# Optimization experiments

Measured on AMD Instinct MI355X. Metric: run time of the kernel, lower is better.

## Reference

```python
import jax, jax.numpy as jnp
import numpy as np

EMBED = 256
HEADS = 8
HEAD_DIM = EMBED // HEADS
K = 7          # kernel_size
DIL = 1        # dilation
PAD = DIL * (K - 1) // 2  # 3
B, H, W = 4, 56, 56


def setup_inputs() -> dict:
    key = jax.random.key(0)
    ks = jax.random.split(key, 9)
    d = {"x": jax.random.normal(ks[0], (B, H, W, EMBED), jnp.float32)}
    for i, name in enumerate(["wq", "wk", "wv", "wo"]):
        d[name] = jax.random.normal(ks[1 + i], (EMBED, EMBED), jnp.float32) * 0.02
    for i, name in enumerate(["bq", "bk", "bv", "bo"]):
        d[name] = jax.random.normal(ks[5 + i], (EMBED,), jnp.float32) * 0.02
    return d


def _unfold(t):
    # t: [N, d, H, W] -> [N, d, K*K, H, W]; zero padding (matches F.unfold),
    # so out-of-bounds neighbors contribute logit 0, NOT -inf (faithful to source).
    h, w = t.shape[2], t.shape[3]
    tp = jnp.pad(t, ((0, 0), (0, 0), (PAD, PAD), (PAD, PAD)))
    patches = [tp[:, :, i * DIL:i * DIL + h, j * DIL:j * DIL + w]
               for i in range(K) for j in range(K)]  # fixed K*K=49 offsets
    return jnp.stack(patches, axis=2)


def reference(x, wq, bq, wk, bk, wv, bv, wo, bo):
    b, h, w, c = x.shape
    scale = HEAD_DIM ** -0.5
    q = x @ wq.T + bq
    k = x @ wk.T + bk
    v = x @ wv.T + bv

    def to_nh(t):  # [B,H,W,C] -> [B*heads, head_dim, H, W]
        return t.reshape(b, h, w, HEADS, HEAD_DIM).transpose(0, 3, 4, 1, 2).reshape(b * HEADS, HEAD_DIM, h, w)

    q, k, v = to_nh(q), to_nh(k), to_nh(v)
    k_unf = _unfold(k)  # [N, d, K2, H, W]
    v_unf = _unfold(v)
    logits = jnp.einsum('ndhw,ndkhw->nkhw', q, k_unf) * scale  # [N, K2, H, W]
    attn = jax.nn.softmax(logits, axis=1)
    out = jnp.einsum('nkhw,ndkhw->ndhw', attn, v_unf)  # [N, d, H, W]
    out = out.reshape(b, HEADS, HEAD_DIM, h, w).transpose(0, 3, 4, 1, 2).reshape(b, h, w, c)
    return out @ wo.T + bo
```

## Files before the change

### kernel.cpp

```cpp
#include <hip/hip_runtime.h>

typedef unsigned int u32;
typedef unsigned short u16;
typedef __attribute__((ext_vector_type(8))) short bf16x8;
typedef __attribute__((ext_vector_type(4))) float f32x4;

#define T_TOK 12544
#define EMB   256
#define IMG   56
#define SCALE 0.17677669529663689f
#define HALO  196
#define KSTR  40
#define VTSTR 224
#define PSTR  232

__device__ __forceinline__ u32 bf16_rtne(float f) {
    u32 u = __builtin_bit_cast(u32, f);
    return (u + 0x7fffu + ((u >> 16) & 1u)) >> 16;
}
__device__ __forceinline__ float bf16_to_f(u32 h) { return __builtin_bit_cast(float, h << 16); }
__device__ __forceinline__ u32 pk2(float a, float b) {
    return bf16_rtne(a) | (bf16_rtne(b) << 16);
}

#define GLD16(g, l) __builtin_amdgcn_global_load_lds( \
    (const __attribute__((address_space(1))) u32*)(g), \
    (__attribute__((address_space(3))) u32*)(l), 16, 0, 0)

__global__ __launch_bounds__(256) void weight_convert(
    const float* __restrict__ wq, const float* __restrict__ wk,
    const float* __restrict__ wv, const float* __restrict__ wo,
    u16* __restrict__ bsh, u16* __restrict__ boh, u16* __restrict__ bol) {
    const int i = blockIdx.x * 256 + threadIdx.x;
    const int w = i >> 14, widx = i & 16383;
    const float* src = (w == 0) ? wq : (w == 1) ? wk : (w == 2) ? wv : wo;
    const float4 f = ((const float4*)src)[widx];
    const float vf[4] = {f.x, f.y, f.z, f.w};
    if (w < 3) {
        ushort4 hv;
        u16* hp = (u16*)&hv;
        #pragma unroll
        for (int c = 0; c < 4; ++c) hp[c] = (u16)bf16_rtne(vf[c]);
        ((ushort4*)bsh)[(w << 14) + widx] = hv;
    } else {
        ushort4 hv, lv;
        u16* hp = (u16*)&hv; u16* lp = (u16*)&lv;
        #pragma unroll
        for (int c = 0; c < 4; ++c) {
            const u32 h = bf16_rtne(vf[c]);
            hp[c] = (u16)h;
            lp[c] = (u16)bf16_rtne(vf[c] - bf16_to_f(h));
        }
        ((ushort4*)boh)[widx] = hv;
        ((ushort4*)bol)[widx] = lv;
    }
}

__global__ __launch_bounds__(256) void qkv_mfma(
    const float* __restrict__ x, const u16* __restrict__ bsh,
    const float* __restrict__ bq, const float* __restrict__ bk, const float* __restrict__ bv,
    u16* __restrict__ qb, u16* __restrict__ kb, u16* __restrict__ vb) {
    __shared__ __attribute__((aligned(16))) u16 sA[128 * 32];
    __shared__ __attribute__((aligned(16))) u16 sB[128 * 32];
    const int nBase = blockIdx.x * 128;
    const int mBase = blockIdx.y * 128;
    const int tid = threadIdx.x, wv = tid >> 6, ln = tid & 63;
    const int lrow = ln & 15, lqd = ln >> 4;
    const int wm = (wv & 1) * 64, wn = (wv >> 1) * 64;
    const int c0 = wv * 128 + ln, r0 = c0 >> 2, kc0 = c0 & 3;
    const int c1 = c0 + 64,       r1 = c1 >> 2, kc1 = c1 & 3;
    const size_t gA0 = (size_t)(mBase + r0) * EMB + kc0 * 8;
    const size_t gA1 = (size_t)(mBase + r1) * EMB + kc1 * 8;
    const size_t gB0 = (size_t)(nBase + r0) * EMB + kc0 * 8;
    const size_t gB1 = (size_t)(nBase + r1) * EMB + kc1 * 8;
    const int l0 = (wv * 128) * 8, l1 = (wv * 128 + 64) * 8;

    f32x4 acc[4][4];
    #pragma unroll
    for (int mi = 0; mi < 4; ++mi)
        #pragma unroll
        for (int ni = 0; ni < 4; ++ni)
            acc[mi][ni] = (f32x4){0.f, 0.f, 0.f, 0.f};

    for (int kt = 0; kt < 8; ++kt) {
        const int k0 = kt * 32;
        GLD16(bsh + gB0 + k0, sB + l0);
        GLD16(bsh + gB1 + k0, sB + l1);
        {
            const float4 f0 = *(const float4*)&x[gA0 + k0];
            const float4 f1 = *(const float4*)&x[gA0 + k0 + 4];
            const uint4 p = {pk2(f0.x, f0.y), pk2(f0.z, f0.w),
                             pk2(f1.x, f1.y), pk2(f1.z, f1.w)};
            *(uint4*)&sA[c0 * 8] = p;
        }
        {
            const float4 f0 = *(const float4*)&x[gA1 + k0];
            const float4 f1 = *(const float4*)&x[gA1 + k0 + 4];
            const uint4 p = {pk2(f0.x, f0.y), pk2(f0.z, f0.w),
                             pk2(f1.x, f1.y), pk2(f1.z, f1.w)};
            *(uint4*)&sA[c1 * 8] = p;
        }
        __syncthreads();
        bf16x8 af[4], bf[4];
        #pragma unroll
        for (int mi = 0; mi < 4; ++mi)
            af[mi] = *(const bf16x8*)&sA[(wm + mi * 16 + lrow) * 32 + lqd * 8];
        #pragma unroll
        for (int ni = 0; ni < 4; ++ni)
            bf[ni] = *(const bf16x8*)&sB[(wn + ni * 16 + lrow) * 32 + lqd * 8];
        #pragma unroll
        for (int mi = 0; mi < 4; ++mi)
            #pragma unroll
            for (int ni = 0; ni < 4; ++ni)
                acc[mi][ni] = __builtin_amdgcn_mfma_f32_16x16x32_bf16(af[mi], bf[ni], acc[mi][ni], 0, 0, 0);
        __syncthreads();
    }

    const int which = nBase >> 8;
    const float* bias = (which == 0) ? bq : (which == 1) ? bk : bv;
    u16* dst = (which == 0) ? qb : (which == 1) ? kb : vb;
    #pragma unroll
    for (int ni = 0; ni < 4; ++ni) {
        const int ncol = nBase + wn + ni * 16 + lrow;
        const int c = ncol & 255;
        const float bz = bias[c];
        #pragma unroll
        for (int mi = 0; mi < 4; ++mi) {
            #pragma unroll
            for (int r = 0; r < 4; ++r) {
                const int row = mBase + wm + mi * 16 + lqd * 4 + r;
                dst[(size_t)row * EMB + c] = (u16)bf16_rtne(acc[mi][ni][r] + bz);
            }
        }
    }
}

__global__ __launch_bounds__(256) void out_mfma(
    const u16* __restrict__ aoh, const u16* __restrict__ aol,
    const u16* __restrict__ boh, const u16* __restrict__ bol,
    const float* __restrict__ bo, float* __restrict__ out) {
    __shared__ __attribute__((aligned(16))) u16 sAh[64 * 32];
    __shared__ __attribute__((aligned(16))) u16 sAl[64 * 32];
    __shared__ __attribute__((aligned(16))) u16 sBh[64 * 32];
    __shared__ __attribute__((aligned(16))) u16 sBl[64 * 32];
    const int nBase = blockIdx.x * 64;
    const int mBase = blockIdx.y * 64;
    const int tid = threadIdx.x, wv = tid >> 6, ln = tid & 63;
    const int lrow = ln & 15, lqd = ln >> 4;
    const int rA = tid >> 2, kcA = tid & 3;
    const size_t gA = (size_t)(mBase + rA) * EMB + kcA * 8;
    const size_t gB = (size_t)(nBase + rA) * EMB + kcA * 8;
    const int lA = wv * 64 * 8;

    f32x4 acc[4];
    #pragma unroll
    for (int mi = 0; mi < 4; ++mi) acc[mi] = (f32x4){0.f, 0.f, 0.f, 0.f};

    for (int kt = 0; kt < 8; ++kt) {
        const int k0 = kt * 32;
        GLD16(aoh + gA + k0, sAh + lA);
        GLD16(aol + gA + k0, sAl + lA);
        GLD16(boh + gB + k0, sBh + lA);
        GLD16(bol + gB + k0, sBl + lA);
        __syncthreads();
        bf16x8 ah[4], al[4];
        #pragma unroll
        for (int mi = 0; mi < 4; ++mi) {
            ah[mi] = *(const bf16x8*)&sAh[(mi * 16 + lrow) * 32 + lqd * 8];
            al[mi] = *(const bf16x8*)&sAl[(mi * 16 + lrow) * 32 + lqd * 8];
        }
        const bf16x8 bh = *(const bf16x8*)&sBh[(wv * 16 + lrow) * 32 + lqd * 8];
        const bf16x8 bl = *(const bf16x8*)&sBl[(wv * 16 + lrow) * 32 + lqd * 8];
        #pragma unroll
        for (int mi = 0; mi < 4; ++mi) {
            acc[mi] = __builtin_amdgcn_mfma_f32_16x16x32_bf16(ah[mi], bh, acc[mi], 0, 0, 0);
            acc[mi] = __builtin_amdgcn_mfma_f32_16x16x32_bf16(al[mi], bh, acc[mi], 0, 0, 0);
            acc[mi] = __builtin_amdgcn_mfma_f32_16x16x32_bf16(ah[mi], bl, acc[mi], 0, 0, 0);
        }
        __syncthreads();
    }

    const int ncol = nBase + wv * 16 + lrow;
    const float bz = bo[ncol];
    #pragma unroll
    for (int mi = 0; mi < 4; ++mi) {
        #pragma unroll
        for (int r = 0; r < 4; ++r) {
            const int row = mBase + mi * 16 + lqd * 4 + r;
            out[(size_t)row * EMB + ncol] = acc[mi][r] + bz;
        }
    }
}

__global__ __launch_bounds__(256, 3) void attn_kernel(
    const u16* __restrict__ qb, const u16* __restrict__ kb, const u16* __restrict__ vb,
    u16* __restrict__ aoh, u16* __restrict__ aol) {
    __shared__ __attribute__((aligned(16))) u16 smem[25088];
    u16* sK  = smem;
    u16* sV1 = smem + 8960;
    u16* sVT = smem + 17920;
    u16* sP  = smem;

    const int tid = threadIdx.x;
    const int w = tid >> 6, ln = tid & 63;
    const int lrow = ln & 15, lqd = ln >> 4;
    const int img = blockIdx.z >> 3, head = blockIdx.z & 7;
    const int ty0 = blockIdx.y * 8, tx0 = blockIdx.x * 8;

    for (int i = tid; i < 1792; i += 256) {
        const int mv = (i >= 896) ? 1 : 0;
        const int ii = i - 896 * mv;
        const int p = ii >> 2, c = ii & 3;
        const int pyh = p / 14, pxh = p - pyh * 14;
        const int gy = ty0 - 3 + pyh, gx = tx0 - 3 + pxh;
        u16* dst = (mv ? sV1 : sK) + p * KSTR + c * 8;
        if (p < HALO && (unsigned)gy < 56u && (unsigned)gx < 56u) {
            const size_t tt = ((size_t)img * IMG + gy) * IMG + gx;
            *(uint4*)dst = *(const uint4*)((mv ? vb : kb) + tt * EMB + head * 32 + c * 8);
        } else {
            *(uint4*)dst = (uint4){0u, 0u, 0u, 0u};
        }
    }
    __syncthreads();

    for (int i = tid; i < 896; i += 256) {
        const int d = i & 31, ho = i >> 5;
        u32 pk[4];
        #pragma unroll
        for (int j = 0; j < 4; ++j) {
            const u32 a = sV1[(ho * 8 + 2 * j)     * KSTR + d];
            const u32 b = sV1[(ho * 8 + 2 * j + 1) * KSTR + d];
            pk[j] = a | (b << 16);
        }
        *(uint4*)&sVT[d * VTSTR + ho * 8] = *(uint4*)pk;
    }

    const int mpix = w * 16 + lrow;
    const int qpy = mpix >> 3, qpx = mpix & 7;
    const size_t qtok = ((size_t)img * IMG + ty0 + qpy) * IMG + tx0 + qpx;
    const bf16x8 aq = *(const bf16x8*)&qb[qtok * EMB + head * 32 + lqd * 8];

    f32x4 ct[13];
    #pragma unroll
    for (int t = 0; t < 13; ++t) ct[t] = (f32x4){0.f, 0.f, 0.f, 0.f};
    #pragma unroll
    for (int t = 0; t < 13; ++t) {
        const bf16x8 bk = *(const bf16x8*)&sK[(t * 16 + lrow) * KSTR + lqd * 8];
        ct[t] = __builtin_amdgcn_mfma_f32_16x16x32_bf16(aq, bk, ct[t], 0, 0, 0);
    }

    int pys[4], pxs[4];
    #pragma unroll
    for (int r = 0; r < 4; ++r) {
        const int row = lqd * 4 + r;
        pys[r] = 2 * w + (row >> 3);
        pxs[r] = row & 7;
    }
    float mr4[4] = {-1e30f, -1e30f, -1e30f, -1e30f};
    #pragma unroll
    for (int t = 0; t < 13; ++t) {
        const int col = t * 16 + lrow;
        const int hy = col / 14, hx = col - 14 * hy;
        const bool okc = (col < HALO);
        #pragma unroll
        for (int r = 0; r < 4; ++r) {
            const bool ok = ((unsigned)(hy - pys[r]) < 7u) &
                            ((unsigned)(hx - pxs[r]) < 7u) & okc;
            const float lv = ok ? ct[t][r] * SCALE : -1e30f;
            ct[t][r] = lv;
            mr4[r] = fmaxf(mr4[r], lv);
        }
    }
    #pragma unroll
    for (int r = 0; r < 4; ++r) {
        float m = mr4[r];
        m = fmaxf(m, __shfl_xor(m, 1));
        m = fmaxf(m, __shfl_xor(m, 2));
        m = fmaxf(m, __shfl_xor(m, 4));
        m = fmaxf(m, __shfl_xor(m, 8));
        mr4[r] = m;
    }
    float sr4[4] = {0.f, 0.f, 0.f, 0.f};
    #pragma unroll
    for (int t = 0; t < 13; ++t)
        #pragma unroll
        for (int r = 0; r < 4; ++r) {
            const float e = __expf(ct[t][r] - mr4[r]);
            ct[t][r] = e;
            sr4[r] += e;
        }
    #pragma unroll
    for (int r = 0; r < 4; ++r) {
        float s = sr4[r];
        s += __shfl_xor(s, 1);
        s += __shfl_xor(s, 2);
        s += __shfl_xor(s, 4);
        s += __shfl_xor(s, 8);
        sr4[r] = 1.0f / s;
    }

    __syncthreads();

    u16* sPw = sP + w * 16 * PSTR;
    #pragma unroll
    for (int t = 0; t < 13; ++t)
        #pragma unroll
        for (int r = 0; r < 4; ++r)
            sPw[(lqd * 4 + r) * PSTR + t * 16 + lrow] = (u16)bf16_rtne(ct[t][r]);
    #pragma unroll
    for (int z = 0; z < 4; ++z) {
        const int idx = z * 64 + ln;
        sPw[(idx >> 4) * PSTR + 208 + (idx & 15)] = 0;
    }

    f32x4 o0 = (f32x4){0.f, 0.f, 0.f, 0.f};
    f32x4 o1 = (f32x4){0.f, 0.f, 0.f, 0.f};
    #pragma unroll
    for (int ks = 0; ks < 7; ++ks) {
        const bf16x8 ap  = *(const bf16x8*)&sPw[lrow * PSTR + ks * 32 + lqd * 8];
        const bf16x8 bv0 = *(const bf16x8*)&sVT[lrow * VTSTR + ks * 32 + lqd * 8];
        const bf16x8 bv1 = *(const bf16x8*)&sVT[(16 + lrow) * VTSTR + ks * 32 + lqd * 8];
        o0 = __builtin_amdgcn_mfma_f32_16x16x32_bf16(ap, bv0, o0, 0, 0, 0);
        o1 = __builtin_amdgcn_mfma_f32_16x16x32_bf16(ap, bv1, o1, 0, 0, 0);
    }

    #pragma unroll
    for (int r = 0; r < 4; ++r) {
        const int row = lqd * 4 + r;
        const int opy = 2 * w + (row >> 3), opx = row & 7;
        const size_t ot = ((size_t)img * IMG + ty0 + opy) * IMG + tx0 + opx;
        const float inv = sr4[r];
        const float v0 = o0[r] * inv;
        const float v1 = o1[r] * inv;
        const size_t base = ot * EMB + head * 32;
        const u32 h0 = bf16_rtne(v0);
        aoh[base + lrow] = (u16)h0;
        aol[base + lrow] = (u16)bf16_rtne(v0 - bf16_to_f(h0));
        const u32 h1 = bf16_rtne(v1);
        aoh[base + 16 + lrow] = (u16)h1;
        aol[base + 16 + lrow] = (u16)bf16_rtne(v1 - bf16_to_f(h1));
    }
}

extern "C" void kernel_launch(void* const* d_in, const int* in_sizes, int n_in,
                              void* d_out, int out_size, void* d_ws, size_t ws_size,
                              hipStream_t stream) {
    const float* x  = (const float*)d_in[0];
    const float* wq = (const float*)d_in[1];
    const float* wk = (const float*)d_in[2];
    const float* wv = (const float*)d_in[3];
    const float* wo = (const float*)d_in[4];
    const float* bq = (const float*)d_in[5];
    const float* bk = (const float*)d_in[6];
    const float* bv = (const float*)d_in[7];
    const float* bo = (const float*)d_in[8];
    float* out = (float*)d_out;

    char* ws = (char*)d_ws;
    u16* qb  = (u16*)(ws);
    u16* kb  = (u16*)(ws +  6422528);
    u16* vb  = (u16*)(ws + 12845056);
    u16* aoh = (u16*)(ws + 19267584);
    u16* aol = (u16*)(ws + 25690112);
    u16* bsh = (u16*)(ws + 32112640);
    u16* boh = (u16*)(ws + 32505856);
    u16* bol = (u16*)(ws + 32636928);

    weight_convert<<<256, 256, 0, stream>>>(wq, wk, wv, wo, bsh, boh, bol);
    qkv_mfma<<<dim3(6, 98), 256, 0, stream>>>(x, bsh, bq, bk, bv, qb, kb, vb);
    attn_kernel<<<dim3(7, 7, 32), 256, 0, stream>>>(qb, kb, vb, aoh, aol);
    out_mfma<<<dim3(4, 196), 256, 0, stream>>>(aoh, aol, boh, bol, bo, out);
}
```

Baseline: 133.8 us.

## Pre-convert x to bf16 and double-buffer GEMM LDS tiles

The convert kernel now also casts x to bf16 into a workspace buffer, so the QKV GEMM can stream A tiles with direct global-to-LDS loads instead of loading fp32 and packing in registers. Both GEMMs use double-buffered shared memory, prefetching the next K-slice while computing the current one, which removes one barrier per iteration. The attention kernel writes V transposed straight into LDS during the halo load, dropping a separate transpose pass and a barrier. The cost is an extra full pass over x (an 6.4MB bf16 write plus its read back) and scattered 16-bit LDS stores for the V transpose.

Result: no change. 134.0 us (+0.2%).

```diff
diff --git a/kernel.cpp b/kernel.cpp
--- a/kernel.cpp
+++ b/kernel.cpp
@@ -19,61 +19,71 @@
     return (u + 0x7fffu + ((u >> 16) & 1u)) >> 16;
 }
 __device__ __forceinline__ float bf16_to_f(u32 h) { return __builtin_bit_cast(float, h << 16); }
-__device__ __forceinline__ u32 pk2(float a, float b) {
-    return bf16_rtne(a) | (bf16_rtne(b) << 16);
-}
 
 #define GLD16(g, l) __builtin_amdgcn_global_load_lds( \
     (const __attribute__((address_space(1))) u32*)(g), \
     (__attribute__((address_space(3))) u32*)(l), 16, 0, 0)
 
-__global__ __launch_bounds__(256) void weight_convert(
-    const float* __restrict__ wq, const float* __restrict__ wk,
+__global__ __launch_bounds__(256) void convert_kernel(
+    const float* __restrict__ x, const float* __restrict__ wq, const float* __restrict__ wk,
     const float* __restrict__ wv, const float* __restrict__ wo,
-    u16* __restrict__ bsh, u16* __restrict__ boh, u16* __restrict__ bol) {
+    u16* __restrict__ xb, u16* __restrict__ bsh,
+    u16* __restrict__ boh, u16* __restrict__ bol) {
     const int i = blockIdx.x * 256 + threadIdx.x;
-    const int w = i >> 14, widx = i & 16383;
-    const float* src = (w == 0) ? wq : (w == 1) ? wk : (w == 2) ? wv : wo;
-    const float4 f = ((const float4*)src)[widx];
-    const float vf[4] = {f.x, f.y, f.z, f.w};
-    if (w < 3) {
+    const int NX4 = T_TOK * EMB / 4;
+    if (i < NX4) {
+        const float4 f = ((const float4*)x)[i];
+        const float vf[4] = {f.x, f.y, f.z, f.w};
         ushort4 hv;
         u16* hp = (u16*)&hv;
         #pragma unroll
         for (int c = 0; c < 4; ++c) hp[c] = (u16)bf16_rtne(vf[c]);
-        ((ushort4*)bsh)[(w << 14) + widx] = hv;
+        ((ushort4*)xb)[i] = hv;
     } else {
-        ushort4 hv, lv;
-        u16* hp = (u16*)&hv; u16* lp = (u16*)&lv;
-        #pragma unroll
-        for (int c = 0; c < 4; ++c) {
-            const u32 h = bf16_rtne(vf[c]);
-            hp[c] = (u16)h;
-            lp[c] = (u16)bf16_rtne(vf[c] - bf16_to_f(h));
-        }
-        ((ushort4*)boh)[widx] = hv;
-        ((ushort4*)bol)[widx] = lv;
+        const int j = i - NX4;
+        const int w = j >> 14, widx = j & 16383;
+        const float* src = (w == 0) ? wq : (w == 1) ? wk : (w == 2) ? wv : wo;
+        const float4 f = ((const float4*)src)[widx];
+        const float vf[4] = {f.x, f.y, f.z, f.w};
+        if (w < 3) {
+            ushort4 hv;
+            u16* hp = (u16*)&hv;
+            #pragma unroll
+            for (int c = 0; c < 4; ++c) hp[c] = (u16)bf16_rtne(vf[c]);
+            ((ushort4*)bsh)[(w << 14) + widx] = hv;
+        } else {
+            ushort4 hv, lv;
+            u16* hp = (u16*)&hv; u16* lp = (u16*)&lv;
+            #pragma unroll
+            for (int c = 0; c < 4; ++c) {
+                const u32 h = bf16_rtne(vf[c]);
+                hp[c] = (u16)h;
+                lp[c] = (u16)bf16_rtne(vf[c] - bf16_to_f(h));
+            }
+            ((ushort4*)boh)[widx] = hv;
+            ((ushort4*)bol)[widx] = lv;
+        }
     }
 }
 
 __global__ __launch_bounds__(256) void qkv_mfma(
-    const float* __restrict__ x, const u16* __restrict__ bsh,
+    const u16* __restrict__ xb, const u16* __restrict__ bsh,
     const float* __restrict__ bq, const float* __restrict__ bk, const float* __restrict__ bv,
     u16* __restrict__ qb, u16* __restrict__ kb, u16* __restrict__ vb) {
-    __shared__ __attribute__((aligned(16))) u16 sA[128 * 32];
-    __shared__ __attribute__((aligned(16))) u16 sB[128 * 32];
+    __shared__ __attribute__((aligned(16))) u16 sA[2][128 * 32];
+    __shared__ __attribute__((aligned(16))) u16 sB[2][128 * 32];
     const int nBase = blockIdx.x * 128;
     const int mBase = blockIdx.y * 128;
-    const int tid = threadIdx.x, wv = tid >> 6, ln = tid & 63;
+    const int tid = threadIdx.x, wv2 = tid >> 6, ln = tid & 63;
     const int lrow = ln & 15, lqd = ln >> 4;
-    const int wm = (wv & 1) * 64, wn = (wv >> 1) * 64;
-    const int c0 = wv * 128 + ln, r0 = c0 >> 2, kc0 = c0 & 3;
-    const int c1 = c0 + 64,       r1 = c1 >> 2, kc1 = c1 & 3;
+    const int wm = (wv2 & 1) * 64, wn = (wv2 >> 1) * 64;
+    const int c0 = wv2 * 128 + ln, r0 = c0 >> 2, kc0 = c0 & 3;
+    const int c1 = c0 + 64,        r1 = c1 >> 2, kc1 = c1 & 3;
     const size_t gA0 = (size_t)(mBase + r0) * EMB + kc0 * 8;
     const size_t gA1 = (size_t)(mBase + r1) * EMB + kc1 * 8;
     const size_t gB0 = (size_t)(nBase + r0) * EMB + kc0 * 8;
     const size_t gB1 = (size_t)(nBase + r1) * EMB + kc1 * 8;
-    const int l0 = (wv * 128) * 8, l1 = (wv * 128 + 64) * 8;
+    const int l0 = (wv2 * 128) * 8, l1 = (wv2 * 128 + 64) * 8;
 
     f32x4 acc[4][4];
     #pragma unroll
@@ -82,38 +92,33 @@
         for (int ni = 0; ni < 4; ++ni)
             acc[mi][ni] = (f32x4){0.f, 0.f, 0.f, 0.f};
 
+    GLD16(xb  + gA0, &sA[0][l0]);
+    GLD16(xb  + gA1, &sA[0][l1]);
+    GLD16(bsh + gB0, &sB[0][l0]);
+    GLD16(bsh + gB1, &sB[0][l1]);
+
     for (int kt = 0; kt < 8; ++kt) {
-        const int k0 = kt * 32;
-        GLD16(bsh + gB0 + k0, sB + l0);
-        GLD16(bsh + gB1 + k0, sB + l1);
-        {
-            const float4 f0 = *(const float4*)&x[gA0 + k0];
-            const float4 f1 = *(const float4*)&x[gA0 + k0 + 4];
-            const uint4 p = {pk2(f0.x, f0.y), pk2(f0.z, f0.w),
-                             pk2(f1.x, f1.y), pk2(f1.z, f1.w)};
-            *(uint4*)&sA[c0 * 8] = p;
-        }
-        {
-            const float4 f0 = *(const float4*)&x[gA1 + k0];
-            const float4 f1 = *(const float4*)&x[gA1 + k0 + 4];
-            const uint4 p = {pk2(f0.x, f0.y), pk2(f0.z, f0.w),
-                             pk2(f1.x, f1.y), pk2(f1.z, f1.w)};
-            *(uint4*)&sA[c1 * 8] = p;
-        }
+        const int b = kt & 1;
         __syncthreads();
+        if (kt < 7) {
+            const int k0 = (kt + 1) * 32;
+            GLD16(xb  + gA0 + k0, &sA[b ^ 1][l0]);
+            GLD16(xb  + gA1 + k0, &sA[b ^ 1][l1]);
+            GLD16(bsh + gB0 + k0, &sB[b ^ 1][l0]);
+            GLD16(bsh + gB1 + k0, &sB[b ^ 1][l1]);
+        }
         bf16x8 af[4], bf[4];
         #pragma unroll
         for (int mi = 0; mi < 4; ++mi)
-            af[mi] = *(const bf16x8*)&sA[(wm + mi * 16 + lrow) * 32 + lqd * 8];
+            af[mi] = *(const bf16x8*)&sA[b][(wm + mi * 16 + lrow) * 32 + lqd * 8];
         #pragma unroll
         for (int ni = 0; ni < 4; ++ni)
-            bf[ni] = *(const bf16x8*)&sB[(wn + ni * 16 + lrow) * 32 + lqd * 8];
+            bf[ni] = *(const bf16x8*)&sB[b][(wn + ni * 16 + lrow) * 32 + lqd * 8];
         #pragma unroll
         for (int mi = 0; mi < 4; ++mi)
             #pragma unroll
             for (int ni = 0; ni < 4; ++ni)
                 acc[mi][ni] = __builtin_amdgcn_mfma_f32_16x16x32_bf16(af[mi], bf[ni], acc[mi][ni], 0, 0, 0);
-        __syncthreads();
     }
 
     const int which = nBase >> 8;
@@ -139,10 +144,10 @@
     const u16* __restrict__ aoh, const u16* __restrict__ aol,
     const u16* __restrict__ boh, const u16* __restrict__ bol,
     const float* __restrict__ bo, float* __restrict__ out) {
-    __shared__ __attribute__((aligned(16))) u16 sAh[64 * 32];
-    __shared__ __attribute__((aligned(16))) u16 sAl[64 * 32];
-    __shared__ __attribute__((aligned(16))) u16 sBh[64 * 32];
-    __shared__ __attribute__((aligned(16))) u16 sBl[64 * 32];
+    __shared__ __attribute__((aligned(16))) u16 sAh[2][64 * 32];
+    __shared__ __attribute__((aligned(16))) u16 sAl[2][64 * 32];
+    __shared__ __attribute__((aligned(16))) u16 sBh[2][64 * 32];
+    __shared__ __attribute__((aligned(16))) u16 sBl[2][64 * 32];
     const int nBase = blockIdx.x * 64;
     const int mBase = blockIdx.y * 64;
     const int tid = threadIdx.x, wv = tid >> 6, ln = tid & 63;
@@ -156,28 +161,35 @@
     #pragma unroll
     for (int mi = 0; mi < 4; ++mi) acc[mi] = (f32x4){0.f, 0.f, 0.f, 0.f};
 
+    GLD16(aoh + gA, &sAh[0][lA]);
+    GLD16(aol + gA, &sAl[0][lA]);
+    GLD16(boh + gB, &sBh[0][lA]);
+    GLD16(bol + gB, &sBl[0][lA]);
+
     for (int kt = 0; kt < 8; ++kt) {
-        const int k0 = kt * 32;
-        GLD16(aoh + gA + k0, sAh + lA);
-        GLD16(aol + gA + k0, sAl + lA);
-        GLD16(boh + gB + k0, sBh + lA);
-        GLD16(bol + gB + k0, sBl + lA);
+        const int b = kt & 1;
         __syncthreads();
+        if (kt < 7) {
+            const int k0 = (kt + 1) * 32;
+            GLD16(aoh + gA + k0, &sAh[b ^ 1][lA]);
+            GLD16(aol + gA + k0, &sAl[b ^ 1][lA]);
+            GLD16(boh + gB + k0, &sBh[b ^ 1][lA]);
+            GLD16(bol + gB + k0, &sBl[b ^ 1][lA]);
+        }
         bf16x8 ah[4], al[4];
         #pragma unroll
         for (int mi = 0; mi < 4; ++mi) {
-            ah[mi] = *(const bf16x8*)&sAh[(mi * 16 + lrow) * 32 + lqd * 8];
-            al[mi] = *(const bf16x8*)&sAl[(mi * 16 + lrow) * 32 + lqd * 8];
-        }
-        const bf16x8 bh = *(const bf16x8*)&sBh[(wv * 16 + lrow) * 32 + lqd * 8];
-        const bf16x8 bl = *(const bf16x8*)&sBl[(wv * 16 + lrow) * 32 + lqd * 8];
+            ah[mi] = *(const bf16x8*)&sAh[b][(mi * 16 + lrow) * 32 + lqd * 8];
+            al[mi] = *(const bf16x8*)&sAl[b][(mi * 16 + lrow) * 32 + lqd * 8];
+        }
+        const bf16x8 bh = *(const bf16x8*)&sBh[b][(wv * 16 + lrow) * 32 + lqd * 8];
+        const bf16x8 bl = *(const bf16x8*)&sBl[b][(wv * 16 + lrow) * 32 + lqd * 8];
         #pragma unroll
         for (int mi = 0; mi < 4; ++mi) {
             acc[mi] = __builtin_amdgcn_mfma_f32_16x16x32_bf16(ah[mi], bh, acc[mi], 0, 0, 0);
             acc[mi] = __builtin_amdgcn_mfma_f32_16x16x32_bf16(al[mi], bh, acc[mi], 0, 0, 0);
             acc[mi] = __builtin_amdgcn_mfma_f32_16x16x32_bf16(ah[mi], bl, acc[mi], 0, 0, 0);
         }
-        __syncthreads();
     }
 
     const int ncol = nBase + wv * 16 + lrow;
@@ -195,11 +207,10 @@
 __global__ __launch_bounds__(256, 3) void attn_kernel(
     const u16* __restrict__ qb, const u16* __restrict__ kb, const u16* __restrict__ vb,
     u16* __restrict__ aoh, u16* __restrict__ aol) {
-    __shared__ __attribute__((aligned(16))) u16 smem[25088];
-    u16* sK  = smem;
-    u16* sV1 = smem + 8960;
-    u16* sVT = smem + 17920;
-    u16* sP  = smem;
+    __shared__ __attribute__((aligned(16))) u16 smem[22016];
+    u16* sVT = smem;
+    u16* sK  = smem + 7168;
+    u16* sP  = smem + 7168;
 
     const int tid = threadIdx.x;
     const int w = tid >> 6, ln = tid & 63;
@@ -213,32 +224,40 @@
         const int p = ii >> 2, c = ii & 3;
         const int pyh = p / 14, pxh = p - pyh * 14;
         const int gy = ty0 - 3 + pyh, gx = tx0 - 3 + pxh;
-        u16* dst = (mv ? sV1 : sK) + p * KSTR + c * 8;
-        if (p < HALO && (unsigned)gy < 56u && (unsigned)gx < 56u) {
-            const size_t tt = ((size_t)img * IMG + gy) * IMG + gx;
-            *(uint4*)dst = *(const uint4*)((mv ? vb : kb) + tt * EMB + head * 32 + c * 8);
+        const bool ok = (p < HALO) & ((unsigned)gy < 56u) & ((unsigned)gx < 56u);
+        if (!mv) {
+            u16* dstk = sK + p * KSTR + c * 8;
+            if (ok) {
+                const size_t tt = ((size_t)img * IMG + gy) * IMG + gx;
+                *(uint4*)dstk = *(const uint4*)(kb + tt * EMB + head * 32 + c * 8);
+            } else {
+                *(uint4*)dstk = (uint4){0u, 0u, 0u, 0u};
+            }
         } else {
-            *(uint4*)dst = (uint4){0u, 0u, 0u, 0u};
-        }
-    }
-    __syncthreads();
-
-    for (int i = tid; i < 896; i += 256) {
-        const int d = i & 31, ho = i >> 5;
-        u32 pk[4];
-        #pragma unroll
-        for (int j = 0; j < 4; ++j) {
-            const u32 a = sV1[(ho * 8 + 2 * j)     * KSTR + d];
-            const u32 b = sV1[(ho * 8 + 2 * j + 1) * KSTR + d];
-            pk[j] = a | (b << 16);
-        }
-        *(uint4*)&sVT[d * VTSTR + ho * 8] = *(uint4*)pk;
+            u16* dv = sVT + (c * 8) * VTSTR + p;
+            if (ok) {
+                const size_t tt = ((size_t)img * IMG + gy) * IMG + gx;
+                const uint4 u = *(const uint4*)(vb + tt * EMB + head * 32 + c * 8);
+                dv[0 * VTSTR] = (u16)(u.x & 0xffffu);
+                dv[1 * VTSTR] = (u16)(u.x >> 16);
+                dv[2 * VTSTR] = (u16)(u.y & 0xffffu);
+                dv[3 * VTSTR] = (u16)(u.y >> 16);
+                dv[4 * VTSTR] = (u16)(u.z & 0xffffu);
+                dv[5 * VTSTR] = (u16)(u.z >> 16);
+                dv[6 * VTSTR] = (u16)(u.w & 0xffffu);
+                dv[7 * VTSTR] = (u16)(u.w >> 16);
+            } else {
+                #pragma unroll
+                for (int j = 0; j < 8; ++j) dv[j * VTSTR] = 0;
+            }
+        }
     }
 
     const int mpix = w * 16 + lrow;
     const int qpy = mpix >> 3, qpx = mpix & 7;
     const size_t qtok = ((size_t)img * IMG + ty0 + qpy) * IMG + tx0 + qpx;
     const bf16x8 aq = *(const bf16x8*)&qb[qtok * EMB + head * 32 + lqd * 8];
+    __syncthreads();
 
     f32x4 ct[13];
     #pragma unroll
@@ -357,17 +376,18 @@
     float* out = (float*)d_out;
 
     char* ws = (char*)d_ws;
-    u16* qb  = (u16*)(ws);
-    u16* kb  = (u16*)(ws +  6422528);
-    u16* vb  = (u16*)(ws + 12845056);
-    u16* aoh = (u16*)(ws + 19267584);
-    u16* aol = (u16*)(ws + 25690112);
-    u16* bsh = (u16*)(ws + 32112640);
-    u16* boh = (u16*)(ws + 32505856);
-    u16* bol = (u16*)(ws + 32636928);
-
-    weight_convert<<<256, 256, 0, stream>>>(wq, wk, wv, wo, bsh, boh, bol);
-    qkv_mfma<<<dim3(6, 98), 256, 0, stream>>>(x, bsh, bq, bk, bv, qb, kb, vb);
+    u16* xb  = (u16*)(ws);
+    u16* qb  = (u16*)(ws +  6422528);
+    u16* kb  = (u16*)(ws + 12845056);
+    u16* vb  = (u16*)(ws + 19267584);
+    u16* aoh = (u16*)(ws + 25690112);
+    u16* aol = (u16*)(ws + 32112640);
+    u16* bsh = (u16*)(ws + 38535168);
+    u16* boh = (u16*)(ws + 38928384);
+    u16* bol = (u16*)(ws + 39059456);
+
+    convert_kernel<<<3392, 256, 0, stream>>>(x, wq, wk, wv, wo, xb, bsh, boh, bol);
+    qkv_mfma<<<dim3(6, 98), 256, 0, stream>>>(xb, bsh, bq, bk, bv, qb, kb, vb);
     attn_kernel<<<dim3(7, 7, 32), 256, 0, stream>>>(qb, kb, vb, aoh, aol);
     out_mfma<<<dim3(4, 196), 256, 0, stream>>>(aoh, aol, boh, bol, bo, out);
 }
```
